# Optimization experiments

Measured on AMD Instinct MI355X. Metric: run time of the kernel, lower is better.

The kernel has to match this reference:

```python
import jax, jax.numpy as jnp
import numpy as np

B, T, V, C, H, HS, L, DFF = 8192, 8, 65, 512, 8, 64, 6, 2048
LN_EPS = 1e-5


def _layernorm(x, g, b):
    mu = jnp.mean(x, axis=-1, keepdims=True)
    var = jnp.mean(jnp.square(x - mu), axis=-1, keepdims=True)
    return (x - mu) * jax.lax.rsqrt(var + LN_EPS) * g + b


def setup_inputs() -> dict:
    key = jax.random.key(0)
    ks = jax.random.split(key, 16)
    s = 0.02
    inp = {
        "idx": jax.random.randint(ks[0], (B, T), 0, V),
        "tok_table": jax.random.normal(ks[1], (V, C), jnp.float32) * s,
        "pos_table": jax.random.normal(ks[2], (T, C), jnp.float32) * s,
        "wq": jax.random.normal(ks[3], (L, H, C, HS), jnp.float32) * s,
        "wk": jax.random.normal(ks[4], (L, H, C, HS), jnp.float32) * s,
        "wv": jax.random.normal(ks[5], (L, H, C, HS), jnp.float32) * s,
        "proj_w": jax.random.normal(ks[6], (L, C, C), jnp.float32) * s,
        "proj_b": jnp.zeros((L, C), jnp.float32),
        "w1": jax.random.normal(ks[7], (L, C, DFF), jnp.float32) * s,
        "b1": jnp.zeros((L, DFF), jnp.float32),
        "w2": jax.random.normal(ks[8], (L, DFF, C), jnp.float32) * s,
        "b2": jnp.zeros((L, C), jnp.float32),
        "ln1_g": jnp.ones((L, C), jnp.float32),
        "ln1_b": jnp.zeros((L, C), jnp.float32),
        "ln2_g": jnp.ones((L, C), jnp.float32),
        "ln2_b": jnp.zeros((L, C), jnp.float32),
        "lm_w": jax.random.normal(ks[9], (C, V), jnp.float32) * s,
        "lm_b": jnp.zeros((V,), jnp.float32),
    }
    return inp


def reference(idx, tok_table, pos_table, wq, wk, wv, proj_w, proj_b,
              w1, b1, w2, b2, ln1_g, ln1_b, ln2_g, ln2_b, lm_w, lm_b):
    idx = idx[:, -T:]
    x = tok_table[idx] + pos_table[None, :T, :]  # [B,T,C]
    mask = jnp.tril(jnp.ones((T, T), bool))
    scale = C ** (-0.5)  # NOTE: original scales by n_embed, not head_size
    for l in range(L):
        q = jnp.einsum('btc,hcd->bhtd', x, wq[l])
        k = jnp.einsum('btc,hcd->bhtd', x, wk[l])
        v = jnp.einsum('btc,hcd->bhtd', x, wv[l])
        att = jnp.einsum('bhtd,bhsd->bhts', q, k) * scale
        att = jnp.where(mask, att, -jnp.inf)
        att = jax.nn.softmax(att, axis=-1)
        o = jnp.einsum('bhts,bhsd->bhtd', att, v)
        o = o.transpose(0, 2, 1, 3).reshape(x.shape[0], T, C)  # concat heads
        o = o @ proj_w[l] + proj_b[l]
        x = _layernorm(x + o, ln1_g[l], ln1_b[l])  # post-norm
        h = jax.nn.relu(x @ w1[l] + b1[l]) @ w2[l] + b2[l]
        x = _layernorm(x + h, ln2_g[l], ln2_b[l])
    logits = x @ lm_w + lm_b  # [B,T,V]
    return logits
```

## Files before the change

kernel.cpp:

```cpp
#include <hip/hip_runtime.h>
#include <hip/hip_bf16.h>
#include <math.h>

#define NTOK  65536
#define CDIM  512
#define NHEAD 8
#define HSZ   64
#define NLAYER 6
#define DFF   2048
#define VOCAB 65

typedef unsigned short u16;
typedef __attribute__((ext_vector_type(8))) __bf16 bf16x8;
typedef __attribute__((ext_vector_type(4))) float f32x4;
typedef __attribute__((ext_vector_type(8))) unsigned short ushort8;

__device__ __forceinline__ float b2f(u16 u) {
    union { unsigned int i; float f; } x; x.i = ((unsigned int)u) << 16; return x.f;
}
__device__ __forceinline__ u16 f2b(float f) {
    union { float f; unsigned int i; } x; x.f = f;
    unsigned int r = x.i + 0x7fffu + ((x.i >> 16) & 1u);
    return (u16)(r >> 16);
}

__device__ __forceinline__ void async16(const u16* g, u16* l) {
    __builtin_amdgcn_global_load_lds(
        (const __attribute__((address_space(1))) void*)g,
        (__attribute__((address_space(3))) void*)l, 16, 0, 0);
}

template<int EPI>
__global__ __launch_bounds__(512)
void gemm_bt(const u16* __restrict__ A, const u16* __restrict__ Bt,
             void* __restrict__ Cout, const float* __restrict__ bias,
             const u16* __restrict__ res, int K, int N, int Nout)
{
    __shared__ u16 lA[2 * 256 * 32];
    __shared__ u16 lB[2 * 128 * 32];
    const int tid  = threadIdx.x;

    const int Nx = gridDim.x;
    const int id = blockIdx.y * Nx + blockIdx.x;
    const int xcd = id & 7;
    const int j0  = id >> 3;
    const int mt  = xcd + 8 * (j0 / Nx);
    const int nt  = j0 - (j0 / Nx) * Nx;
    const int m0  = mt * 256;
    const int n0  = nt * 128;

    const int lane = tid & 63;
    const int wv   = tid >> 6;
    const int wr   = (wv >> 1) * 64;
    const int wc   = (wv & 1) * 64;
    const int r16  = lane & 15;
    const int quad = lane >> 4;

    f32x4 acc[4][4] = {};

    const int srow = tid >> 2, skseg = (tid & 3) * 8;
    const u16* pA  = A  + (size_t)(m0 + srow) * K + skseg;
    const u16* pA2 = pA + (size_t)128 * K;
    const u16* pB  = Bt + (size_t)(n0 + srow) * K + skseg;
    u16* lAt = &lA[(size_t)tid * 8];
    u16* lBt = &lB[(size_t)tid * 8];

    async16(pA,  lAt);
    async16(pA2, lAt + 4096);
    async16(pB,  lBt);
    __syncthreads();

    int s = 0;
    for (int k0 = 0; k0 < K; k0 += 32) {
        if (k0 + 32 < K) {
            const int sn = (s ^ 1);
            async16(pA  + k0 + 32, lAt + sn * 8192);
            async16(pA2 + k0 + 32, lAt + sn * 8192 + 4096);
            async16(pB  + k0 + 32, lBt + sn * 4096);
        }
        const u16* bA = &lA[s * 8192];
        const u16* bB = &lB[s * 4096];
        bf16x8 af[4], bfr[4];
#pragma unroll
        for (int i = 0; i < 4; i++)
            af[i] = *(const bf16x8*)(const void*)&bA[(wr + i * 16 + r16) * 32 + quad * 8];
#pragma unroll
        for (int j = 0; j < 4; j++)
            bfr[j] = *(const bf16x8*)(const void*)&bB[(wc + j * 16 + r16) * 32 + quad * 8];
#pragma unroll
        for (int j = 0; j < 4; j++)
#pragma unroll
            for (int i = 0; i < 4; i++)
                acc[j][i] = __builtin_amdgcn_mfma_f32_16x16x32_bf16(bfr[j], af[i], acc[j][i], 0, 0, 0);
        __syncthreads();
        s ^= 1;
    }

#pragma unroll
    for (int i = 0; i < 4; i++) {
        const int row = m0 + wr + i * 16 + r16;
#pragma unroll
        for (int j = 0; j < 4; j++) {
            const int colb = n0 + wc + j * 16 + quad * 4;
            float v[4];
#pragma unroll
            for (int r = 0; r < 4; r++) v[r] = acc[j][i][r];
            if (EPI == 1 || EPI == 2) {
                const f32x4 b4 = *(const f32x4*)(const void*)&bias[colb];
#pragma unroll
                for (int r = 0; r < 4; r++) v[r] += b4[r];
            }
            if (EPI == 1) {
                const uint2 rv = *(const uint2*)(const void*)&res[(size_t)row * N + colb];
                v[0] += b2f((u16)(rv.x & 0xffffu));
                v[1] += b2f((u16)(rv.x >> 16));
                v[2] += b2f((u16)(rv.y & 0xffffu));
                v[3] += b2f((u16)(rv.y >> 16));
            }
            if (EPI == 2) {
#pragma unroll
                for (int r = 0; r < 4; r++) v[r] = fmaxf(v[r], 0.f);
            }
            if (EPI == 3) {
#pragma unroll
                for (int r = 0; r < 4; r++) {
                    const int col = colb + r;
                    if (col < Nout)
                        ((float*)Cout)[(size_t)row * Nout + col] = v[r] + bias[col];
                }
            } else {
                uint2 o;
                o.x = (unsigned)f2b(v[0]) | ((unsigned)f2b(v[1]) << 16);
                o.y = (unsigned)f2b(v[2]) | ((unsigned)f2b(v[3]) << 16);
                *(uint2*)(void*)&((u16*)Cout)[(size_t)row * N + colb] = o;
            }
        }
    }
}

__global__ __launch_bounds__(256)
void attn_k(const u16* __restrict__ qkv, u16* __restrict__ out)
{
    __shared__ float sq[4][8][64], sk[4][8][64], sv[4][8][64], sp[4][64];
    const int w = threadIdx.x >> 6, lane = threadIdx.x & 63;
    const int unit = blockIdx.x * 4 + w;
    const int b = unit >> 3, h = unit & 7;
    const size_t base = (size_t)b * 8 * 1536 + h * 64;
#pragma unroll
    for (int t = 0; t < 8; t++) {
        sq[w][t][lane] = b2f(qkv[base + t * 1536 + lane]);
        sk[w][t][lane] = b2f(qkv[base + t * 1536 + 512 + lane]);
        sv[w][t][lane] = b2f(qkv[base + t * 1536 + 1024 + lane]);
    }
    __syncthreads();
    const int t = lane >> 3, s = lane & 7;
    float sc = -1e30f;
    if (s <= t) {
        float d = 0.f;
#pragma unroll
        for (int c = 0; c < 64; c++) d += sq[w][t][c] * sk[w][s][c];
        sc = d * 0.04419417382415922f;
    }
    float mx = sc;
#pragma unroll
    for (int m = 1; m < 8; m <<= 1) mx = fmaxf(mx, __shfl_xor(mx, m, 8));
    float e = __expf(sc - mx);
    if (s > t) e = 0.f;
    float sum = e;
#pragma unroll
    for (int m = 1; m < 8; m <<= 1) sum += __shfl_xor(sum, m, 8);
    sp[w][lane] = e / sum;
    __syncthreads();
#pragma unroll
    for (int tt = 0; tt < 8; tt++) {
        float a = 0.f;
#pragma unroll
        for (int ss = 0; ss < 8; ss++) a += sp[w][tt * 8 + ss] * sv[w][ss][lane];
        out[((size_t)b * 8 + tt) * 512 + h * 64 + lane] = f2b(a);
    }
}

__global__ __launch_bounds__(256)
void ln_k(const u16* __restrict__ y, const float* __restrict__ g,
          const float* __restrict__ be, u16* __restrict__ x)
{
    const int w = threadIdx.x >> 6, lane = threadIdx.x & 63;
    const size_t tok = (size_t)blockIdx.x * 4 + w;
    const u16* row = y + tok * 512 + lane * 8;
    ushort8 raw = *(const ushort8*)(const void*)row;
    float v[8];
#pragma unroll
    for (int i = 0; i < 8; i++) v[i] = b2f(raw[i]);
    float s = 0.f;
#pragma unroll
    for (int i = 0; i < 8; i++) s += v[i];
#pragma unroll
    for (int m = 1; m < 64; m <<= 1) s += __shfl_xor(s, m, 64);
    const float mu = s * (1.f / 512.f);
    float q = 0.f;
#pragma unroll
    for (int i = 0; i < 8; i++) { float d = v[i] - mu; q += d * d; }
#pragma unroll
    for (int m = 1; m < 64; m <<= 1) q += __shfl_xor(q, m, 64);
    const float inv = rsqrtf(q * (1.f / 512.f) + 1e-5f);
    f32x4 g0  = *(const f32x4*)(const void*)&g[lane * 8];
    f32x4 g1  = *(const f32x4*)(const void*)&g[lane * 8 + 4];
    f32x4 b0  = *(const f32x4*)(const void*)&be[lane * 8];
    f32x4 b1v = *(const f32x4*)(const void*)&be[lane * 8 + 4];
    ushort8 o;
#pragma unroll
    for (int i = 0; i < 4; i++) o[i]     = f2b((v[i] - mu) * inv * g0[i] + b0[i]);
#pragma unroll
    for (int i = 0; i < 4; i++) o[i + 4] = f2b((v[i + 4] - mu) * inv * g1[i] + b1v[i]);
    *(ushort8*)(void*)&x[tok * 512 + lane * 8] = o;
}

__global__ __launch_bounds__(256)
void embed_k(const int* __restrict__ idx, const float* __restrict__ tokt,
             const float* __restrict__ pos, u16* __restrict__ xb)
{
    const int tk = blockIdx.x;
    const int t = tk & 7;
    const int ix = idx[tk];
    const int c = threadIdx.x;
    const size_t o = (size_t)tk * 512;
    xb[o + c]       = f2b(tokt[(size_t)ix * 512 + c]       + pos[t * 512 + c]);
    xb[o + c + 256] = f2b(tokt[(size_t)ix * 512 + c + 256] + pos[t * 512 + c + 256]);
}

__global__ __launch_bounds__(256)
void conv_t2_k(const float* __restrict__ in, u16* __restrict__ out, int K, int N)
{
    __shared__ float t[32][33];
    const int tx = threadIdx.x & 31, ty4 = (threadIdx.x >> 5) * 4;
    const int n0 = blockIdx.x * 32, k0 = blockIdx.y * 32, l = blockIdx.z;
    const size_t per = (size_t)K * N;
    const float* src = in + l * per;
#pragma unroll
    for (int r = 0; r < 4; r++)
        t[ty4 + r][tx] = src[(size_t)(k0 + ty4 + r) * N + n0 + tx];
    __syncthreads();
    u16* dst = out + l * per;
#pragma unroll
    for (int r = 0; r < 4; r++)
        dst[(size_t)(n0 + ty4 + r) * K + k0 + tx] = f2b(t[tx][ty4 + r]);
}

__global__ __launch_bounds__(256)
void conv_qkv2_k(const float* __restrict__ wq, const float* __restrict__ wk,
                 const float* __restrict__ wv, u16* __restrict__ out)
{
    __shared__ float t[32][33];
    const int tx = threadIdx.x & 31, ty4 = (threadIdx.x >> 5) * 4;
    const int c0 = blockIdx.x * 32, d0 = blockIdx.y * 32;
    const int z = blockIdx.z;
    const int sel = z / 48, rem = z - sel * 48;
    const int l = rem >> 3, h = rem & 7;
    const float* src = (sel == 0) ? wq : (sel == 1) ? wk : wv;
    const float* sb = src + (((size_t)l * 8 + h) * 512) * 64;
#pragma unroll
    for (int r = 0; r < 4; r++)
        t[ty4 + r][tx] = sb[(size_t)(c0 + ty4 + r) * 64 + d0 + tx];
    __syncthreads();
    u16* dst = out + (size_t)l * 786432 + (size_t)(sel * 512 + h * 64 + d0) * 512;
#pragma unroll
    for (int r = 0; r < 4; r++)
        dst[(size_t)(ty4 + r) * 512 + c0 + tx] = f2b(t[tx][ty4 + r]);
}

__global__ __launch_bounds__(256)
void conv_lm_k(const float* __restrict__ lm_w, u16* __restrict__ out)
{
    int gid = blockIdx.x * 256 + threadIdx.x;
    int n = gid >> 9, c = gid & 511;
    out[gid] = (n < VOCAB) ? f2b(lm_w[(size_t)c * VOCAB + n]) : (u16)0;
}

extern "C" void kernel_launch(void* const* d_in, const int* in_sizes, int n_in,
                              void* d_out, int out_size, void* d_ws, size_t ws_size,
                              hipStream_t stream)
{
    const int*   idx    = (const int*)  d_in[0];
    const float* tokt   = (const float*)d_in[1];
    const float* post   = (const float*)d_in[2];
    const float* wq     = (const float*)d_in[3];
    const float* wk     = (const float*)d_in[4];
    const float* wvp    = (const float*)d_in[5];
    const float* proj_w = (const float*)d_in[6];
    const float* proj_b = (const float*)d_in[7];
    const float* w1     = (const float*)d_in[8];
    const float* b1     = (const float*)d_in[9];
    const float* w2     = (const float*)d_in[10];
    const float* b2     = (const float*)d_in[11];
    const float* ln1_g  = (const float*)d_in[12];
    const float* ln1_b  = (const float*)d_in[13];
    const float* ln2_g  = (const float*)d_in[14];
    const float* ln2_b  = (const float*)d_in[15];
    const float* lm_w   = (const float*)d_in[16];
    const float* lm_b   = (const float*)d_in[17];
    float* out = (float*)d_out;

    char* ws = (char*)d_ws;
    u16* wqkvt = (u16*)(ws + 0);
    u16* wprjt = (u16*)(ws + 9437184);
    u16* ww1t  = (u16*)(ws + 12582912);
    u16* ww2t  = (u16*)(ws + 25165824);
    u16* wlmt  = (u16*)(ws + 37748736);
    u16* xb    = (u16*)(ws + 37879808);
    char* big  = ws + 104988672;

    const size_t fixed_bytes = 104988672ull;
    int chunk = 4096;
    const int cands[4] = {65536, 32768, 16384, 8192};
    for (int i = 0; i < 4; i++) {
        if (fixed_bytes + (size_t)cands[i] * 4096ull <= ws_size) { chunk = cands[i]; break; }
    }
    const int nchunks = NTOK / chunk;
    u16* qkvc  = (u16*)big;
    u16* attnc = (u16*)(big + (size_t)chunk * 3072);
    u16* h1c   = (u16*)big;

    conv_qkv2_k<<<dim3(16, 2, 144), 256, 0, stream>>>(wq, wk, wvp, wqkvt);
    conv_t2_k  <<<dim3(16, 16, 6), 256, 0, stream>>>(proj_w, wprjt, 512, 512);
    conv_t2_k  <<<dim3(64, 16, 6), 256, 0, stream>>>(w1, ww1t, 512, 2048);
    conv_t2_k  <<<dim3(16, 64, 6), 256, 0, stream>>>(w2, ww2t, 2048, 512);
    conv_lm_k  <<<128 * 512 / 256, 256, 0, stream>>>(lm_w, wlmt);

    embed_k<<<NTOK, 256, 0, stream>>>(idx, tokt, post, xb);

    for (int l = 0; l < NLAYER; l++) {
        for (int c = 0; c < nchunks; c++) {
            const size_t t0 = (size_t)c * chunk;
            gemm_bt<0><<<dim3(12, chunk / 256), 512, 0, stream>>>(
                xb + t0 * 512, wqkvt + (size_t)l * 786432, qkvc,
                nullptr, nullptr, 512, 1536, 1536);
            attn_k<<<chunk / 4, 256, 0, stream>>>(qkvc, attnc);
            gemm_bt<1><<<dim3(4, chunk / 256), 512, 0, stream>>>(
                attnc, wprjt + (size_t)l * 262144, xb + t0 * 512,
                proj_b + l * 512, xb + t0 * 512, 512, 512, 512);
        }
        ln_k<<<NTOK / 4, 256, 0, stream>>>(xb, ln1_g + l * 512, ln1_b + l * 512, xb);
        for (int c = 0; c < nchunks; c++) {
            const size_t t0 = (size_t)c * chunk;
            gemm_bt<2><<<dim3(16, chunk / 256), 512, 0, stream>>>(
                xb + t0 * 512, ww1t + (size_t)l * 1048576, h1c,
                b1 + l * 2048, nullptr, 512, 2048, 2048);
            gemm_bt<1><<<dim3(4, chunk / 256), 512, 0, stream>>>(
                h1c, ww2t + (size_t)l * 1048576, xb + t0 * 512,
                b2 + l * 512, xb + t0 * 512, 2048, 512, 512);
        }
        ln_k<<<NTOK / 4, 256, 0, stream>>>(xb, ln2_g + l * 512, ln2_b + l * 512, xb);
    }

    gemm_bt<3><<<dim3(1, 256), 512, 0, stream>>>(
        xb, wlmt, out, lm_b, nullptr, 512, 128, VOCAB);
}
```

Measured before the change: 4.468 ms.

## Drop GEMM double buffering for K=64 steps, vectorize attention and embed

The GEMM main loop switches from a double-buffered K=32 pipeline, where the next tile's async loads overlapped the current MFMAs, to a single-stage loop that loads a K=64 tile, synchronizes, and computes both halves. This halves the number of barriers per K but removes load/compute overlap within a block. The attention kernel now loads Q/K/V with 16-byte vector loads, pads shared arrays to 65 to avoid bank conflicts, and writes 8 outputs per lane with a vector store. The embed kernel is vectorized to 8 elements per thread with far fewer blocks.

```diff
diff --git a/kernel.cpp b/kernel.cpp
--- a/kernel.cpp
+++ b/kernel.cpp
@@ -65,35 +65,33 @@
     u16* lAt = &lA[(size_t)tid * 8];
     u16* lBt = &lB[(size_t)tid * 8];
 
-    async16(pA,  lAt);
-    async16(pA2, lAt + 4096);
-    async16(pB,  lBt);
-    __syncthreads();
-
-    int s = 0;
-    for (int k0 = 0; k0 < K; k0 += 32) {
-        if (k0 + 32 < K) {
-            const int sn = (s ^ 1);
-            async16(pA  + k0 + 32, lAt + sn * 8192);
-            async16(pA2 + k0 + 32, lAt + sn * 8192 + 4096);
-            async16(pB  + k0 + 32, lBt + sn * 4096);
-        }
-        const u16* bA = &lA[s * 8192];
-        const u16* bB = &lB[s * 4096];
-        bf16x8 af[4], bfr[4];
-#pragma unroll
-        for (int i = 0; i < 4; i++)
-            af[i] = *(const bf16x8*)(const void*)&bA[(wr + i * 16 + r16) * 32 + quad * 8];
-#pragma unroll
-        for (int j = 0; j < 4; j++)
-            bfr[j] = *(const bf16x8*)(const void*)&bB[(wc + j * 16 + r16) * 32 + quad * 8];
-#pragma unroll
-        for (int j = 0; j < 4; j++)
+    for (int k0 = 0; k0 < K; k0 += 64) {
+        async16(pA  + k0,      lAt);
+        async16(pA2 + k0,      lAt + 4096);
+        async16(pA  + k0 + 32, lAt + 8192);
+        async16(pA2 + k0 + 32, lAt + 12288);
+        async16(pB  + k0,      lBt);
+        async16(pB  + k0 + 32, lBt + 4096);
+        __syncthreads();
+
+#pragma unroll
+        for (int s = 0; s < 2; s++) {
+            const u16* bA = &lA[s * 8192];
+            const u16* bB = &lB[s * 4096];
+            bf16x8 af[4], bfr[4];
 #pragma unroll
             for (int i = 0; i < 4; i++)
-                acc[j][i] = __builtin_amdgcn_mfma_f32_16x16x32_bf16(bfr[j], af[i], acc[j][i], 0, 0, 0);
+                af[i] = *(const bf16x8*)(const void*)&bA[(wr + i * 16 + r16) * 32 + quad * 8];
+#pragma unroll
+            for (int j = 0; j < 4; j++)
+                bfr[j] = *(const bf16x8*)(const void*)&bB[(wc + j * 16 + r16) * 32 + quad * 8];
+#pragma unroll
+            for (int j = 0; j < 4; j++)
+#pragma unroll
+                for (int i = 0; i < 4; i++)
+                    acc[j][i] = __builtin_amdgcn_mfma_f32_16x16x32_bf16(bfr[j], af[i], acc[j][i], 0, 0, 0);
+        }
         __syncthreads();
-        s ^= 1;
     }
 
 #pragma unroll
@@ -141,16 +139,22 @@
 __global__ __launch_bounds__(256)
 void attn_k(const u16* __restrict__ qkv, u16* __restrict__ out)
 {
-    __shared__ float sq[4][8][64], sk[4][8][64], sv[4][8][64], sp[4][64];
+    __shared__ float sq[4][8][65], sk[4][8][65], sv[4][8][65], sp[4][64];
     const int w = threadIdx.x >> 6, lane = threadIdx.x & 63;
     const int unit = blockIdx.x * 4 + w;
     const int b = unit >> 3, h = unit & 7;
     const size_t base = (size_t)b * 8 * 1536 + h * 64;
-#pragma unroll
-    for (int t = 0; t < 8; t++) {
-        sq[w][t][lane] = b2f(qkv[base + t * 1536 + lane]);
-        sk[w][t][lane] = b2f(qkv[base + t * 1536 + 512 + lane]);
-        sv[w][t][lane] = b2f(qkv[base + t * 1536 + 1024 + lane]);
+    {
+        const int t = lane >> 3, d0 = (lane & 7) * 8;
+        const ushort8 q8 = *(const ushort8*)(const void*)&qkv[base + t * 1536 + d0];
+        const ushort8 k8 = *(const ushort8*)(const void*)&qkv[base + t * 1536 + 512 + d0];
+        const ushort8 v8 = *(const ushort8*)(const void*)&qkv[base + t * 1536 + 1024 + d0];
+#pragma unroll
+        for (int i = 0; i < 8; i++) {
+            sq[w][t][d0 + i] = b2f(q8[i]);
+            sk[w][t][d0 + i] = b2f(k8[i]);
+            sv[w][t][d0 + i] = b2f(v8[i]);
+        }
     }
     __syncthreads();
     const int t = lane >> 3, s = lane & 7;
@@ -171,12 +175,19 @@
     for (int m = 1; m < 8; m <<= 1) sum += __shfl_xor(sum, m, 8);
     sp[w][lane] = e / sum;
     __syncthreads();
-#pragma unroll
-    for (int tt = 0; tt < 8; tt++) {
-        float a = 0.f;
-#pragma unroll
-        for (int ss = 0; ss < 8; ss++) a += sp[w][tt * 8 + ss] * sv[w][ss][lane];
-        out[((size_t)b * 8 + tt) * 512 + h * 64 + lane] = f2b(a);
+    {
+        const int tt = lane >> 3, d0 = (lane & 7) * 8;
+        float a[8] = {};
+#pragma unroll
+        for (int ss = 0; ss < 8; ss++) {
+            const float p = sp[w][tt * 8 + ss];
+#pragma unroll
+            for (int i = 0; i < 8; i++) a[i] += p * sv[w][ss][d0 + i];
+        }
+        ushort8 o;
+#pragma unroll
+        for (int i = 0; i < 8; i++) o[i] = f2b(a[i]);
+        *(ushort8*)(void*)&out[((size_t)b * 8 + tt) * 512 + h * 64 + d0] = o;
     }
 }
 
@@ -219,13 +230,20 @@
 void embed_k(const int* __restrict__ idx, const float* __restrict__ tokt,
              const float* __restrict__ pos, u16* __restrict__ xb)
 {
-    const int tk = blockIdx.x;
+    const int gid = blockIdx.x * 256 + threadIdx.x;
+    const int tk = gid >> 6, seg = (gid & 63) * 8;
     const int t = tk & 7;
     const int ix = idx[tk];
-    const int c = threadIdx.x;
-    const size_t o = (size_t)tk * 512;
-    xb[o + c]       = f2b(tokt[(size_t)ix * 512 + c]       + pos[t * 512 + c]);
-    xb[o + c + 256] = f2b(tokt[(size_t)ix * 512 + c + 256] + pos[t * 512 + c + 256]);
+    const f32x4 a0 = *(const f32x4*)(const void*)&tokt[(size_t)ix * 512 + seg];
+    const f32x4 a1 = *(const f32x4*)(const void*)&tokt[(size_t)ix * 512 + seg + 4];
+    const f32x4 p0 = *(const f32x4*)(const void*)&pos[t * 512 + seg];
+    const f32x4 p1 = *(const f32x4*)(const void*)&pos[t * 512 + seg + 4];
+    ushort8 o;
+#pragma unroll
+    for (int i = 0; i < 4; i++) o[i]     = f2b(a0[i] + p0[i]);
+#pragma unroll
+    for (int i = 0; i < 4; i++) o[i + 4] = f2b(a1[i] + p1[i]);
+    *(ushort8*)(void*)&xb[(size_t)tk * 512 + seg] = o;
 }
 
 __global__ __launch_bounds__(256)
@@ -326,7 +344,7 @@
     conv_t2_k  <<<dim3(16, 64, 6), 256, 0, stream>>>(w2, ww2t, 2048, 512);
     conv_lm_k  <<<128 * 512 / 256, 256, 0, stream>>>(lm_w, wlmt);
 
-    embed_k<<<NTOK, 256, 0, stream>>>(idx, tokt, post, xb);
+    embed_k<<<NTOK * 64 / 256, 256, 0, stream>>>(idx, tokt, post, xb);
 
     for (int l = 0; l < NLAYER; l++) {
         for (int c = 0; c < nchunks; c++) {
```

Measured after the change: 4.069 ms. -8.9%, faster.
